# Kernel tuning notes

Measured on AMD Instinct MI355X. Metric: run time of the kernel, lower is better.

Reference implementation:

```python
import jax, jax.numpy as jnp
import numpy as np

L, V, D = 8, 512, 256            # num_loci, per-locus vocab, embedding_dim
B, K = 8192, 16                  # batch, candidates per sample
HID = 2 * D                      # pooling MLP hidden width


def setup_inputs() -> dict:
    key = jax.random.key(0)
    k_tok, k_tab, k_w1, k_w2 = jax.random.split(key, 4)
    haplotypes = jax.random.randint(k_tok, (B, K, L), 0, V, dtype=jnp.int64)
    # nn.Embedding default init: N(0, 1); padding_idx row zeroed.
    tables = jax.random.normal(k_tab, (L, V, D), dtype=jnp.float32)
    tables = tables.at[:, 0, :].set(0.0)
    # Xavier-uniform for the two Linear layers (stored as [in, out]).
    lim1 = float(np.sqrt(6.0 / (L * D + HID)))
    W1 = jax.random.uniform(k_w1, (L * D, HID), jnp.float32, -lim1, lim1)
    b1 = jnp.zeros((HID,), jnp.float32)
    lim2 = float(np.sqrt(6.0 / (HID + D)))
    W2 = jax.random.uniform(k_w2, (HID, D), jnp.float32, -lim2, lim2)
    b2 = jnp.zeros((D,), jnp.float32)
    return {"haplotypes": haplotypes, "tables": tables,
            "W1": W1, "b1": b1, "W2": W2, "b2": b2}


def reference(haplotypes, tables, W1, b1, W2, b2):
    b, k, num_loci = haplotypes.shape
    vocab = tables.shape[1]
    tok = jnp.clip(haplotypes.reshape(-1, num_loci), 0, vocab - 1)  # [N, L]
    # Per-locus gather, vectorized over loci: [N, L, D]
    emb = tables[jnp.arange(num_loci), tok]
    # padding_idx row is all-zeros; masking keeps forward identical and
    # matches torch's zero-gradient behavior for the padding row.
    emb = emb * (tok != 0)[..., None].astype(emb.dtype)
    x = emb.reshape(emb.shape[0], num_loci * tables.shape[2])  # concat -> [N, L*D]
    h = jax.nn.gelu(x @ W1 + b1, approximate=False)            # torch GELU = erf
    out = h @ W2 + b2                                          # [N, D]
    return out.reshape(b, k, tables.shape[2])
```

## Files before the change

kernel.cpp:

```cpp
#include <hip/hip_runtime.h>
#include <math.h>

typedef __attribute__((ext_vector_type(8))) short  short8;
typedef __attribute__((ext_vector_type(4))) float  floatx4;
typedef __attribute__((ext_vector_type(2))) float  float2v;
typedef __attribute__((ext_vector_type(4))) unsigned int uintx4;

#define NLOCI 8
#define VOCAB 512
#define DDIM  256
#define HID   512
#define NSAMP (8192 * 16)

__device__ __forceinline__ float bitsf(unsigned int u) {
    union { unsigned int u; float f; } c; c.u = u; return c.f;
}
__device__ __forceinline__ unsigned short f2bf(float f) {
    union { float f; unsigned int u; } c; c.f = f;
    unsigned int u = c.u;
    return (unsigned short)((u + 0x7FFFu + ((u >> 16) & 1u)) >> 16);
}
__device__ __forceinline__ unsigned short f2bf_fast(float f) {
    union { float f; unsigned int u; } c; c.f = f;
    return (unsigned short)((c.u + 0x8000u) >> 16);
}
__device__ __forceinline__ float gelu_fast(float x) {
    float t = x * x;
    float y = x * __builtin_fmaf(0.035677408f, t, 0.79788456f);
    float e = __builtin_amdgcn_exp2f(y * 2.8853901f);
    float r = __builtin_amdgcn_rcpf(e + 1.0f);
    return x - x * r;
}
__device__ __forceinline__ void async_copy16(const void* g, void* l) {
    __builtin_amdgcn_global_load_lds(
        (const __attribute__((address_space(1))) unsigned int*)g,
        (__attribute__((address_space(3))) unsigned int*)l, 16, 0, 0);
}

__device__ __forceinline__ short8 sum_gelu(const uintx4* g) {
    short8 afrag;
#pragma unroll
    for (int j = 0; j < 4; ++j) {
        float2v u0 = (float2v){bitsf(g[0][j] << 16), bitsf(g[0][j] & 0xFFFF0000u)};
        float2v u1 = (float2v){bitsf(g[1][j] << 16), bitsf(g[1][j] & 0xFFFF0000u)};
        float2v u2 = (float2v){bitsf(g[2][j] << 16), bitsf(g[2][j] & 0xFFFF0000u)};
        float2v u3 = (float2v){bitsf(g[3][j] << 16), bitsf(g[3][j] & 0xFFFF0000u)};
        float2v u4 = (float2v){bitsf(g[4][j] << 16), bitsf(g[4][j] & 0xFFFF0000u)};
        float2v u5 = (float2v){bitsf(g[5][j] << 16), bitsf(g[5][j] & 0xFFFF0000u)};
        float2v u6 = (float2v){bitsf(g[6][j] << 16), bitsf(g[6][j] & 0xFFFF0000u)};
        float2v u7 = (float2v){bitsf(g[7][j] << 16), bitsf(g[7][j] & 0xFFFF0000u)};
        float2v sj = ((u0 + u1) + (u2 + u3)) + ((u4 + u5) + (u6 + u7));
        afrag[2 * j]     = (short)f2bf_fast(gelu_fast(sj[0]));
        afrag[2 * j + 1] = (short)f2bf_fast(gelu_fast(sj[1]));
    }
    return afrag;
}

__global__ __launch_bounds__(256) void k_prep(
    const float* __restrict__ tables,
    const float* __restrict__ W1,
    const float* __restrict__ b1,
    const float* __restrict__ W2,
    unsigned short* __restrict__ Tp,
    unsigned short* __restrict__ W2t)
{
    __shared__ unsigned short a_lds[64 * 256];
    __shared__ unsigned short bt_lds[64 * 256];

    const int t = threadIdx.x;

    if (blockIdx.x >= 512) {
        const int bid = blockIdx.x - 512;
        const int r0 = (bid & 7) * 64;
        const int c0 = (bid >> 3) * 64;
        float* tile = (float*)a_lds;
#pragma unroll
        for (int i = 0; i < 16; ++i) {
            int flat = i * 256 + t;
            int rr = flat >> 6, cc = flat & 63;
            tile[rr * 65 + cc] = W2[(r0 + rr) * DDIM + c0 + cc];
        }
        __syncthreads();
#pragma unroll
        for (int i = 0; i < 8; ++i) {
            int flat = i * 256 + t;
            int cc = flat >> 5, rp = (flat & 31) * 2;
            ushort2 v;
            v.x = f2bf(tile[rp * 65 + cc]);
            v.y = f2bf(tile[(rp + 1) * 65 + cc]);
            *(ushort2*)(W2t + (c0 + cc) * HID + r0 + rp) = v;
        }
        return;
    }

    const int l  = blockIdx.x >> 6;
    const int v0 = ((blockIdx.x >> 3) & 7) * 64;
    const int n0 = (blockIdx.x & 7) * 64;

    {
        const float* asrc = tables + (l * 512 + v0) * 256;
#pragma unroll
        for (int i = 0; i < 16; ++i) {
            int flat = i * 1024 + t * 4;
            int row = flat >> 8, k = flat & 255;
            float4 v = *(const float4*)(asrc + flat);
            ushort4 pk4;
            pk4.x = f2bf(v.x); pk4.y = f2bf(v.y); pk4.z = f2bf(v.z); pk4.w = f2bf(v.w);
            int chunkX = (k >> 3) ^ (row & 31);
            *(ushort4*)(a_lds + row * 256 + chunkX * 8 + (k & 7)) = pk4;
        }
    }
    {
        const int n = t & 63;
        const int kq = (t >> 6) * 64;
        const float* bsrc = W1 + (l * 256) * 512 + n0 + n;
#pragma unroll
        for (int i = 0; i < 8; ++i) {
            int k0 = kq + i * 8;
            short8 pk8;
#pragma unroll
            for (int j = 0; j < 8; ++j)
                pk8[j] = (short)f2bf(bsrc[(k0 + j) * 512]);
            int chunkX = (k0 >> 3) ^ (n & 31);
            *(short8*)(bt_lds + n * 256 + chunkX * 8) = pk8;
        }
    }
    __syncthreads();

    const int wave = t >> 6, lane = t & 63;
    const int p = lane & 15, q = lane >> 4;
    const int arow = wave * 16 + p;

    floatx4 acc[4];
#pragma unroll
    for (int nt = 0; nt < 4; ++nt) acc[nt] = (floatx4){0.f, 0.f, 0.f, 0.f};

#pragma unroll
    for (int kc = 0; kc < 8; ++kc) {
        int cq = kc * 4 + q;
        short8 afrag = *(const short8*)(a_lds + arow * 256 + (cq ^ (arow & 31)) * 8);
#pragma unroll
        for (int nt = 0; nt < 4; ++nt) {
            int brow = nt * 16 + p;
            short8 bfrag = *(const short8*)(bt_lds + brow * 256 + (cq ^ (brow & 31)) * 8);
            acc[nt] = __builtin_amdgcn_mfma_f32_16x16x32_bf16(afrag, bfrag, acc[nt], 0, 0, 0);
        }
    }

#pragma unroll
    for (int nt = 0; nt < 4; ++nt) {
        int col = n0 + nt * 16 + p;
        float badd = (l == 0) ? b1[col] : 0.0f;
#pragma unroll
        for (int r = 0; r < 4; ++r) {
            int row = v0 + wave * 16 + q * 4 + r;
            Tp[(l * 512 + row) * 512 + col] = f2bf(acc[nt][r] + badd);
        }
    }
}

__global__ __launch_bounds__(256, 4) void k_main(
    const int* __restrict__ hap,
    const unsigned short* __restrict__ Tp,
    const unsigned short* __restrict__ W2t,
    const float* __restrict__ b2,
    float* __restrict__ out)
{
    __shared__ unsigned short w2_lds[256 * 64];

    const int t = threadIdx.x;
    const int wave = t >> 6, lane = t & 63;
    const int p = lane & 15, q = lane >> 4;
    const int m_base = blockIdx.x * 64 + wave * 16;

    unsigned int goff[8];
    {
        const uintx4* hp = (const uintx4*)(hap + (m_base + p) * 8);
        uintx4 h0 = hp[0], h1 = hp[1];
#pragma unroll
        for (int l = 0; l < 4; ++l) {
            goff[l]     = (unsigned)(l)     * 524288u + (h0[l] & 511u) * 1024u + (unsigned)(q * 32);
            goff[l + 4] = (unsigned)(l + 4) * 524288u + (h1[l] & 511u) * 1024u + (unsigned)(q * 32);
        }
    }
    const char* Tpc = (const char*)Tp;

    const int drow = lane >> 3;
    const int jx = (lane & 7) ^ (drow & 7);
    const int c_src = (((jx << 1) | (jx >> 2)) & 7);
    const unsigned short* wsrc = W2t + (wave * 64 + drow) * 512 + c_src * 8;
    const int p7 = p & 7;

    floatx4 acc[16];
#pragma unroll
    for (int nt = 0; nt < 16; ++nt) acc[nt] = (floatx4){0.f, 0.f, 0.f, 0.f};

    uintx4 gbuf[8];
#pragma unroll
    for (int l = 0; l < 8; ++l)
        gbuf[l] = *(const uintx4*)(Tpc + goff[l]);
    __builtin_amdgcn_sched_barrier(0);

#pragma unroll
    for (int kb = 0; kb < 8; ++kb) {
        asm volatile("s_waitcnt lgkmcnt(0)" ::: "memory");
        __builtin_amdgcn_s_barrier();
        __builtin_amdgcn_sched_barrier(0);
#pragma unroll
        for (int i = 0; i < 8; ++i)
            async_copy16(wsrc + kb * 64 + i * 8 * 512,
                         w2_lds + (wave * 64 + i * 8) * 64);
        __builtin_amdgcn_sched_barrier(0);

        asm volatile("s_waitcnt vmcnt(8)" ::: "memory");
        short8 afrag0 = sum_gelu(gbuf);
        __builtin_amdgcn_sched_barrier(0);

#pragma unroll
        for (int l = 0; l < 8; ++l)
            gbuf[l] = *(const uintx4*)(Tpc + goff[l] + kb * 128 + 16);
        __builtin_amdgcn_sched_barrier(0);

        asm volatile("s_waitcnt vmcnt(8)" ::: "memory");
        __builtin_amdgcn_s_barrier();
        __builtin_amdgcn_sched_barrier(0);

        {
            const unsigned short* b0 = w2_lds + p * 64 + ((q ^ p7) * 8);
            __builtin_amdgcn_s_setprio(1);
#pragma unroll
            for (int nt = 0; nt < 16; ++nt) {
                short8 bfrag = *(const short8*)(b0 + nt * 1024);
                acc[nt] = __builtin_amdgcn_mfma_f32_16x16x32_bf16(afrag0, bfrag, acc[nt], 0, 0, 0);
            }
            __builtin_amdgcn_s_setprio(0);
        }

        asm volatile("s_waitcnt vmcnt(0)" ::: "memory");
        short8 afrag1 = sum_gelu(gbuf);
        __builtin_amdgcn_sched_barrier(0);

        if (kb < 7) {
#pragma unroll
            for (int l = 0; l < 8; ++l)
                gbuf[l] = *(const uintx4*)(Tpc + goff[l] + (kb + 1) * 128);
            __builtin_amdgcn_sched_barrier(0);
        }

        {
            const unsigned short* b1p = w2_lds + p * 64 + (((4 + q) ^ p7) * 8);
            __builtin_amdgcn_s_setprio(1);
#pragma unroll
            for (int nt = 0; nt < 16; ++nt) {
                short8 bfrag = *(const short8*)(b1p + nt * 1024);
                acc[nt] = __builtin_amdgcn_mfma_f32_16x16x32_bf16(afrag1, bfrag, acc[nt], 0, 0, 0);
            }
            __builtin_amdgcn_s_setprio(0);
        }
    }

#pragma unroll
    for (int nt = 0; nt < 16; ++nt) {
        int n = nt * 16 + p;
        float b2v = b2[n];
#pragma unroll
        for (int r = 0; r < 4; ++r) {
            int m = m_base + q * 4 + r;
            __builtin_nontemporal_store(acc[nt][r] + b2v, out + m * 256 + n);
        }
    }
}

extern "C" void kernel_launch(void* const* d_in, const int* in_sizes, int n_in,
                              void* d_out, int out_size, void* d_ws, size_t ws_size,
                              hipStream_t stream) {
    const int*   hap    = (const int*)d_in[0];
    const float* tables = (const float*)d_in[1];
    const float* W1     = (const float*)d_in[2];
    const float* b1     = (const float*)d_in[3];
    const float* W2     = (const float*)d_in[4];
    const float* b2     = (const float*)d_in[5];
    float*       outp   = (float*)d_out;

    unsigned short* Tp  = (unsigned short*)d_ws;
    unsigned short* W2t = (unsigned short*)d_ws + NLOCI * VOCAB * HID;

    k_prep<<<dim3(544), dim3(256), 0, stream>>>(tables, W1, b1, W2, Tp, W2t);
    k_main<<<dim3(NSAMP / 64), dim3(256), 0, stream>>>(hap, Tp, W2t, b2, outp);
}
```

Measured before the change: 307.3 us.

## Split fused gather-GELU-GEMM into separate gather kernel and bf16 GEMM kernel

Replaces the single fused kernel with two kernels. The first gathers the eight per-locus rows of precomputed layer-1 outputs, sums them, applies GELU, and writes a bf16 hidden matrix into the output buffer. The second is a plain LDS-tiled MFMA GEMM that streams both the hidden tile and the second-layer weights through LDS. This separates the latency-bound random gathers from the matrix-core work so each can be scheduled on its own terms. The cost is a full extra write and read of the hidden activations through global memory. It also relies on each GEMM block reading only the hidden rows it later overwrites, which makes aliasing the output buffer safe.

```diff
diff --git a/kernel.cpp b/kernel.cpp
--- a/kernel.cpp
+++ b/kernel.cpp
@@ -159,101 +159,77 @@
     }
 }
 
-__global__ __launch_bounds__(256, 4) void k_main(
+__global__ __launch_bounds__(256) void k_gather(
     const int* __restrict__ hap,
     const unsigned short* __restrict__ Tp,
+    unsigned short* __restrict__ H)
+{
+    const int wid  = (int)((blockIdx.x * 256 + threadIdx.x) >> 6);
+    const int lane = threadIdx.x & 63;
+    const char* Tpc = (const char*)Tp;
+    const int* hp = hap + wid * 8;
+
+    uintx4 g[8];
+#pragma unroll
+    for (int l = 0; l < 8; ++l) {
+        unsigned tok = ((unsigned)hp[l]) & 511u;
+        g[l] = *(const uintx4*)(Tpc + (unsigned)l * 524288u + tok * 1024u
+                                + (unsigned)(lane * 16));
+    }
+    short8 hv = sum_gelu(g);
+    *(short8*)(H + wid * 512 + lane * 8) = hv;
+}
+
+__global__ __launch_bounds__(256, 4) void k_gemm(
+    const unsigned short* H,
     const unsigned short* __restrict__ W2t,
     const float* __restrict__ b2,
-    float* __restrict__ out)
+    float* out)
 {
-    __shared__ unsigned short w2_lds[256 * 64];
+    __shared__ unsigned short b_lds[256 * 64];
+    __shared__ unsigned short a_lds[64 * 64];
 
     const int t = threadIdx.x;
     const int wave = t >> 6, lane = t & 63;
     const int p = lane & 15, q = lane >> 4;
-    const int m_base = blockIdx.x * 64 + wave * 16;
-
-    unsigned int goff[8];
-    {
-        const uintx4* hp = (const uintx4*)(hap + (m_base + p) * 8);
-        uintx4 h0 = hp[0], h1 = hp[1];
-#pragma unroll
-        for (int l = 0; l < 4; ++l) {
-            goff[l]     = (unsigned)(l)     * 524288u + (h0[l] & 511u) * 1024u + (unsigned)(q * 32);
-            goff[l + 4] = (unsigned)(l + 4) * 524288u + (h1[l] & 511u) * 1024u + (unsigned)(q * 32);
-        }
-    }
-    const char* Tpc = (const char*)Tp;
+    const int m_blk = blockIdx.x * 64;
 
     const int drow = lane >> 3;
-    const int jx = (lane & 7) ^ (drow & 7);
-    const int c_src = (((jx << 1) | (jx >> 2)) & 7);
-    const unsigned short* wsrc = W2t + (wave * 64 + drow) * 512 + c_src * 8;
+    const int jx   = (lane & 7) ^ (drow & 7);
+    const unsigned short* bsrc = W2t + (wave * 64 + drow) * 512 + jx * 8;
+    const unsigned short* asrc = H + (m_blk + wave * 16 + drow) * 512 + jx * 8;
     const int p7 = p & 7;
 
     floatx4 acc[16];
 #pragma unroll
     for (int nt = 0; nt < 16; ++nt) acc[nt] = (floatx4){0.f, 0.f, 0.f, 0.f};
 
-    uintx4 gbuf[8];
-#pragma unroll
-    for (int l = 0; l < 8; ++l)
-        gbuf[l] = *(const uintx4*)(Tpc + goff[l]);
-    __builtin_amdgcn_sched_barrier(0);
-
-#pragma unroll
     for (int kb = 0; kb < 8; ++kb) {
         asm volatile("s_waitcnt lgkmcnt(0)" ::: "memory");
         __builtin_amdgcn_s_barrier();
         __builtin_amdgcn_sched_barrier(0);
 #pragma unroll
         for (int i = 0; i < 8; ++i)
-            async_copy16(wsrc + kb * 64 + i * 8 * 512,
-                         w2_lds + (wave * 64 + i * 8) * 64);
-        __builtin_amdgcn_sched_barrier(0);
-
-        asm volatile("s_waitcnt vmcnt(8)" ::: "memory");
-        short8 afrag0 = sum_gelu(gbuf);
-        __builtin_amdgcn_sched_barrier(0);
-
-#pragma unroll
-        for (int l = 0; l < 8; ++l)
-            gbuf[l] = *(const uintx4*)(Tpc + goff[l] + kb * 128 + 16);
-        __builtin_amdgcn_sched_barrier(0);
-
-        asm volatile("s_waitcnt vmcnt(8)" ::: "memory");
+            async_copy16(bsrc + kb * 64 + i * 8 * 512,
+                         b_lds + (wave * 64 + i * 8) * 64);
+#pragma unroll
+        for (int i = 0; i < 2; ++i)
+            async_copy16(asrc + kb * 64 + i * 8 * 512,
+                         a_lds + (wave * 16 + i * 8) * 64);
+        asm volatile("s_waitcnt vmcnt(0)" ::: "memory");
         __builtin_amdgcn_s_barrier();
         __builtin_amdgcn_sched_barrier(0);
 
-        {
-            const unsigned short* b0 = w2_lds + p * 64 + ((q ^ p7) * 8);
+#pragma unroll
+        for (int s = 0; s < 2; ++s) {
+            const int slot = (s * 4 + q) ^ p7;
+            short8 afrag = *(const short8*)(a_lds + (wave * 16 + p) * 64 + slot * 8);
+            const unsigned short* bb = b_lds + p * 64 + slot * 8;
             __builtin_amdgcn_s_setprio(1);
 #pragma unroll
             for (int nt = 0; nt < 16; ++nt) {
-                short8 bfrag = *(const short8*)(b0 + nt * 1024);
-                acc[nt] = __builtin_amdgcn_mfma_f32_16x16x32_bf16(afrag0, bfrag, acc[nt], 0, 0, 0);
-            }
-            __builtin_amdgcn_s_setprio(0);
-        }
-
-        asm volatile("s_waitcnt vmcnt(0)" ::: "memory");
-        short8 afrag1 = sum_gelu(gbuf);
-        __builtin_amdgcn_sched_barrier(0);
-
-        if (kb < 7) {
-#pragma unroll
-            for (int l = 0; l < 8; ++l)
-                gbuf[l] = *(const uintx4*)(Tpc + goff[l] + (kb + 1) * 128);
-            __builtin_amdgcn_sched_barrier(0);
-        }
-
-        {
-            const unsigned short* b1p = w2_lds + p * 64 + (((4 + q) ^ p7) * 8);
-            __builtin_amdgcn_s_setprio(1);
-#pragma unroll
-            for (int nt = 0; nt < 16; ++nt) {
-                short8 bfrag = *(const short8*)(b1p + nt * 1024);
-                acc[nt] = __builtin_amdgcn_mfma_f32_16x16x32_bf16(afrag1, bfrag, acc[nt], 0, 0, 0);
+                short8 bfrag = *(const short8*)(bb + nt * 1024);
+                acc[nt] = __builtin_amdgcn_mfma_f32_16x16x32_bf16(afrag, bfrag, acc[nt], 0, 0, 0);
             }
             __builtin_amdgcn_s_setprio(0);
         }
@@ -265,7 +241,7 @@
         float b2v = b2[n];
 #pragma unroll
         for (int r = 0; r < 4; ++r) {
-            int m = m_base + q * 4 + r;
+            int m = m_blk + wave * 16 + q * 4 + r;
             __builtin_nontemporal_store(acc[nt][r] + b2v, out + m * 256 + n);
         }
     }
@@ -284,7 +260,9 @@
 
     unsigned short* Tp  = (unsigned short*)d_ws;
     unsigned short* W2t = (unsigned short*)d_ws + NLOCI * VOCAB * HID;
+    unsigned short* Hbf = (unsigned short*)d_out;
 
     k_prep<<<dim3(544), dim3(256), 0, stream>>>(tables, W1, b1, W2, Tp, W2t);
-    k_main<<<dim3(NSAMP / 64), dim3(256), 0, stream>>>(hap, Tp, W2t, b2, outp);
-}
+    k_gather<<<dim3(NSAMP * 64 / 256), dim3(256), 0, stream>>>(hap, Tp, Hbf);
+    k_gemm<<<dim3(NSAMP / 64), dim3(256), 0, stream>>>(Hbf, W2t, b2, outp);
+}
```

Measured after the change: 263.4 us. 1.17x faster.
